# Kernel tuning notes

Hardware: AMD Instinct MI355X
Metric: run time of the kernel (lower is better)

The kernel has to match this reference:

```python
import jax, jax.numpy as jnp
import numpy as np

B, L, D = 8, 1024, 1024
H = 16
DPH = D // H  # 64
MAX_REL = 32  # relative position clip; vocab = 2*MAX_REL+1 (use_neg_dist=True)


def setup_inputs() -> dict:
    key = jax.random.key(0)
    ks = jax.random.split(key, 12)
    s = 1.0 / np.sqrt(D)
    return {
        "key": jax.random.normal(ks[0], (B, L, D), jnp.float32),
        "value": jax.random.normal(ks[1], (B, L, D), jnp.float32),
        "query": jax.random.normal(ks[2], (B, L, D), jnp.float32),
        "Wq": jax.random.normal(ks[3], (D, D), jnp.float32) * s,
        "bq": jnp.zeros((D,), jnp.float32),
        "Wk": jax.random.normal(ks[4], (D, D), jnp.float32) * s,
        "bk": jnp.zeros((D,), jnp.float32),
        "Wv": jax.random.normal(ks[5], (D, D), jnp.float32) * s,
        "bv": jnp.zeros((D,), jnp.float32),
        "Wo": jax.random.normal(ks[6], (D, D), jnp.float32) * s,
        "bo": jnp.zeros((D,), jnp.float32),
        "rel_emb": jax.random.normal(ks[7], (2 * MAX_REL + 1, DPH), jnp.float32) * 0.02,
    }


def reference(key, value, query, Wq, bq, Wk, bk, Wv, bv, Wo, bo, rel_emb):
    # shape: [B, L, D] -> [B, H, L, DPH]
    def shape(x):
        return x.reshape(B, L, H, DPH).transpose(0, 2, 1, 3)

    q = shape(query @ Wq.T + bq) / np.float32(np.sqrt(DPH))
    k = shape(key @ Wk.T + bk)
    v = shape(value @ Wv.T + bv)

    # relative position indices, clipped to [-MAX_REL, MAX_REL], shifted to [0, 2*MAX_REL]
    r = jnp.arange(L)
    dist = jnp.clip(r[None, :] - r[:, None], -MAX_REL, MAX_REL) + MAX_REL  # [L, L]
    rel = rel_emb[dist]  # [L, L, DPH]; same table for keys and values

    # scores = QK^T + Q . rel_keys  (relative_matmul with transpose=True)
    scores = jnp.einsum('bhqd,bhkd->bhqk', q, k) + jnp.einsum('bhqd,qkd->bhqk', q, rel)
    attn = jax.nn.softmax(scores.astype(jnp.float32), axis=-1).astype(q.dtype)

    # context = attn @ V + attn . rel_values (relative_matmul with transpose=False)
    ctx = jnp.einsum('bhqk,bhkd->bhqd', attn, v) + jnp.einsum('bhqk,qkd->bhqd', attn, rel)
    ctx = ctx.transpose(0, 2, 1, 3).reshape(B, L, D)
    out = ctx @ Wo.T + bo
    return out, attn
```

## Files before the change

### kernel.cpp

```cpp
#include <hip/hip_runtime.h>

typedef unsigned short u16;
typedef _Float16 f16;
typedef __attribute__((ext_vector_type(8))) _Float16 f16x8;
typedef __attribute__((ext_vector_type(4))) _Float16 f16x4;
typedef __attribute__((ext_vector_type(2))) _Float16 f16x2;
typedef __attribute__((ext_vector_type(4))) float f32x4;

#define MFMA16(acc, a, b) acc = __builtin_amdgcn_mfma_f32_16x16x32_f16(a, b, acc, 0, 0, 0)

__device__ __forceinline__ void gl2lds16(const void* g, void* l) {
  __builtin_amdgcn_global_load_lds(
      (const __attribute__((address_space(1))) void*)g,
      (__attribute__((address_space(3))) void*)l, 16, 0, 0);
}

__device__ __forceinline__ void cvt8(const float* __restrict__ src, f16* __restrict__ dst, int i) {
  const float* p = src + (size_t)i * 8;
  f32x4 a = *(const f32x4*)p;
  f32x4 b = *(const f32x4*)(p + 4);
  f16x8 o;
#pragma unroll
  for (int j = 0; j < 4; j++) {
    o[j] = (f16)a[j];
    o[j + 4] = (f16)b[j];
  }
  *(f16x8*)(dst + (size_t)i * 8) = o;
}

__global__ __launch_bounds__(256) void cvt_all(const float* __restrict__ Wq, const float* __restrict__ Wk,
                                               const float* __restrict__ Wv, const float* __restrict__ Wo,
                                               const float* __restrict__ rel, f16* __restrict__ f0,
                                               f16* __restrict__ f1, f16* __restrict__ f2,
                                               f16* __restrict__ f3, f16* __restrict__ fr) {
  const int NW = 131072;
  int i = blockIdx.x * 256 + threadIdx.x;
  if (i < NW) cvt8(Wq, f0, i);
  else if (i < 2 * NW) cvt8(Wk, f1, i - NW);
  else if (i < 3 * NW) cvt8(Wv, f2, i - 2 * NW);
  else if (i < 4 * NW) cvt8(Wo, f3, i - 3 * NW);
  else if (i < 4 * NW + 520) cvt8(rel, fr, i - 4 * NW);
}

__global__ __launch_bounds__(256) void gemm_qkv(const float* __restrict__ Aq, const float* __restrict__ Ak,
                                                const float* __restrict__ Av, const f16* __restrict__ W0,
                                                const f16* __restrict__ W1, const f16* __restrict__ W2,
                                                const float* __restrict__ b0, const float* __restrict__ b1,
                                                const float* __restrict__ b2, f16* __restrict__ O0,
                                                f16* __restrict__ O1, f16* __restrict__ O2) {
  int id = blockIdx.x;
  int which = id >> 9;
  int iid = id & 511;
  const float* A = (which == 0) ? Aq : (which == 1) ? Ak : Av;
  const f16* Wt = (which == 0) ? W0 : (which == 1) ? W1 : W2;
  const float* bias = (which == 0) ? b0 : (which == 1) ? b1 : b2;
  f16* out = (which == 0) ? O0 : (which == 1) ? O1 : O2;
  float scale = (which == 0) ? 0.125f : 1.0f;

  int m0 = (iid >> 3) << 7;
  int n0 = (iid & 7) << 7;
  int tid = threadIdx.x;
  int w = tid >> 6, lane = tid & 63, c = lane & 15, g = lane >> 4;
  int wm = (w >> 1) << 6, wn = (w & 1) << 6;

  __shared__ f16 As[128 * 32];
  __shared__ f16 Bs[128 * 32];

  f32x4 acc[4][4] = {};
  int ci0 = tid, ci1 = tid + 256;
  int r0 = ci0 >> 2, ks0 = (ci0 & 3) << 3;
  int r1 = ci1 >> 2, ks1 = (ci1 & 3) << 3;

  for (int k0 = 0; k0 < 1024; k0 += 32) {
    __syncthreads();
    gl2lds16(Wt + (size_t)(n0 + (ci0 >> 2)) * 1024 + k0 + ((ci0 & 3) << 3), Bs + w * 512);
    gl2lds16(Wt + (size_t)(n0 + (ci1 >> 2)) * 1024 + k0 + ((ci1 & 3) << 3), Bs + w * 512 + 2048);
    {
      const float* ap0 = A + (size_t)(m0 + r0) * 1024 + k0 + ks0;
      const float* ap1 = A + (size_t)(m0 + r1) * 1024 + k0 + ks1;
      f32x4 x0 = *(const f32x4*)ap0, x1 = *(const f32x4*)(ap0 + 4);
      f32x4 y0 = *(const f32x4*)ap1, y1 = *(const f32x4*)(ap1 + 4);
      f16x8 h0, h1;
#pragma unroll
      for (int j = 0; j < 4; j++) {
        h0[j] = (f16)x0[j];
        h0[j + 4] = (f16)x1[j];
        h1[j] = (f16)y0[j];
        h1[j + 4] = (f16)y1[j];
      }
      *(f16x8*)(As + (r0 << 5) + ks0) = h0;
      *(f16x8*)(As + (r1 << 5) + ks1) = h1;
    }
    __syncthreads();
    f16x8 af[4], bf[4];
#pragma unroll
    for (int mf = 0; mf < 4; mf++) af[mf] = *(const f16x8*)(As + ((wm + mf * 16 + c) << 5) + (g << 3));
#pragma unroll
    for (int nf = 0; nf < 4; nf++) bf[nf] = *(const f16x8*)(Bs + ((wn + nf * 16 + c) << 5) + (g << 3));
#pragma unroll
    for (int mf = 0; mf < 4; mf++)
#pragma unroll
      for (int nf = 0; nf < 4; nf++) MFMA16(acc[mf][nf], af[mf], bf[nf]);
  }

#pragma unroll
  for (int mf = 0; mf < 4; mf++)
#pragma unroll
    for (int nf = 0; nf < 4; nf++) {
      int row0 = m0 + wm + mf * 16 + (g << 2);
      int col = n0 + wn + nf * 16 + c;
      if (which == 2) {
        f16x4 vv;
#pragma unroll
        for (int r = 0; r < 4; r++) vv[r] = (f16)(acc[mf][nf][r] + bias[col]);
        size_t idx = (size_t)((row0 >> 10) * 16 + (col >> 6)) * 65536 + (size_t)(col & 63) * 1024 + (row0 & 1023);
        *(f16x4*)(out + idx) = vv;
      } else {
#pragma unroll
        for (int r = 0; r < 4; r++) {
          int row = row0 + r;
          size_t idx = (size_t)((row >> 10) * 16 + (col >> 6)) * 65536 + ((row & 1023) << 6) + (col & 63);
          out[idx] = (f16)((acc[mf][nf][r] + bias[col]) * scale);
        }
      }
    }
}

__global__ __launch_bounds__(256) void gemm_out(const f16* __restrict__ A, const f16* __restrict__ Wt,
                                                const float* __restrict__ bias, float* __restrict__ out) {
  int id = blockIdx.x;
  int m0 = (id >> 3) << 7;
  int n0 = (id & 7) << 7;
  int tid = threadIdx.x;
  int w = tid >> 6, lane = tid & 63, c = lane & 15, g = lane >> 4;
  int wm = (w >> 1) << 6, wn = (w & 1) << 6;

  __shared__ f16 As[128 * 32];
  __shared__ f16 Bs[128 * 32];

  f32x4 acc[4][4] = {};
  int ci0 = tid, ci1 = tid + 256;

  for (int k0 = 0; k0 < 1024; k0 += 32) {
    __syncthreads();
    gl2lds16(A + (size_t)(m0 + (ci0 >> 2)) * 1024 + k0 + ((ci0 & 3) << 3), As + w * 512);
    gl2lds16(A + (size_t)(m0 + (ci1 >> 2)) * 1024 + k0 + ((ci1 & 3) << 3), As + w * 512 + 2048);
    gl2lds16(Wt + (size_t)(n0 + (ci0 >> 2)) * 1024 + k0 + ((ci0 & 3) << 3), Bs + w * 512);
    gl2lds16(Wt + (size_t)(n0 + (ci1 >> 2)) * 1024 + k0 + ((ci1 & 3) << 3), Bs + w * 512 + 2048);
    __syncthreads();
    f16x8 af[4], bf[4];
#pragma unroll
    for (int mf = 0; mf < 4; mf++) af[mf] = *(const f16x8*)(As + ((wm + mf * 16 + c) << 5) + (g << 3));
#pragma unroll
    for (int nf = 0; nf < 4; nf++) bf[nf] = *(const f16x8*)(Bs + ((wn + nf * 16 + c) << 5) + (g << 3));
#pragma unroll
    for (int mf = 0; mf < 4; mf++)
#pragma unroll
      for (int nf = 0; nf < 4; nf++) MFMA16(acc[mf][nf], af[mf], bf[nf]);
  }

#pragma unroll
  for (int mf = 0; mf < 4; mf++)
#pragma unroll
    for (int nf = 0; nf < 4; nf++)
#pragma unroll
      for (int r = 0; r < 4; r++) {
        int row = m0 + wm + mf * 16 + (g << 2) + r;
        int col = n0 + wn + nf * 16 + c;
        out[(size_t)row * 1024 + col] = acc[mf][nf][r] + bias[col];
      }
}

__global__ __launch_bounds__(256) void attn_fused(const f16* __restrict__ Q, const f16* __restrict__ Km,
                                                  const f16* __restrict__ Vt, const f16* __restrict__ rel,
                                                  float* __restrict__ attn, f16* __restrict__ ctx) {
  int id = blockIdx.x;
  int sw = ((id & 7) << 10) + (id >> 3);
  int bh = sw >> 6;
  int q0 = (sw & 63) << 4;
  int b = bh >> 4, h = bh & 15;
  int tid = threadIdx.x;
  int w = tid >> 6, lane = tid & 63, c = lane & 15, g = lane >> 4;

  __shared__ float qrel_s[16 * 68];
  __shared__ float rmax[4][16], rsum[4][16], rlo[4][16], rhi[4][16];
  __shared__ float lo_s[16], hi_s[16];
  __shared__ f16 Pq[16][1032];
  __shared__ f16 rel_s[65 * 64];

  const f16* Qb = Q + ((size_t)bh << 16);
  const f16* Kb = Km + ((size_t)bh << 16);
  const f16* Vtb = Vt + ((size_t)bh << 16);

  for (int i = tid; i < 65 * 64; i += 256) rel_s[i] = rel[i];

  f16x8 aq0 = *(const f16x8*)(Qb + ((q0 + c) << 6) + (g << 3));
  f16x8 aq1 = *(const f16x8*)(Qb + ((q0 + c) << 6) + 32 + (g << 3));

  if (w == 0) {
#pragma unroll
    for (int tf = 0; tf < 5; tf++) {
      int t = tf * 16 + c;
      int tc = (t < 65) ? t : 0;
      f32x4 ar = {};
      f16x8 b0 = *(const f16x8*)(rel + (tc << 6) + (g << 3));
      f16x8 b1 = *(const f16x8*)(rel + (tc << 6) + 32 + (g << 3));
      MFMA16(ar, aq0, b0);
      MFMA16(ar, aq1, b1);
      if (t < 65) {
#pragma unroll
        for (int r = 0; r < 4; r++) qrel_s[((g << 2) + r) * 68 + t] = ar[r];
      }
    }
  }
  __syncthreads();

  float s[16][4];
  int kbase = w << 8;
#pragma unroll
  for (int f = 0; f < 16; f++) {
    int kcol = kbase + (f << 4) + c;
    f32x4 a4 = {};
    f16x8 b0 = *(const f16x8*)(Kb + (kcol << 6) + (g << 3));
    f16x8 b1 = *(const f16x8*)(Kb + (kcol << 6) + 32 + (g << 3));
    MFMA16(a4, aq0, b0);
    MFMA16(a4, aq1, b1);
#pragma unroll
    for (int r = 0; r < 4; r++) {
      int rowl = (g << 2) + r;
      int d = kcol - (q0 + rowl);
      int t = (d < -32 ? -32 : (d > 32 ? 32 : d)) + 32;
      s[f][r] = a4[r] + qrel_s[rowl * 68 + t];
    }
  }

  float m[4] = {-3.0e38f, -3.0e38f, -3.0e38f, -3.0e38f};
#pragma unroll
  for (int f = 0; f < 16; f++)
#pragma unroll
    for (int r = 0; r < 4; r++) m[r] = fmaxf(m[r], s[f][r]);
#pragma unroll
  for (int mk = 1; mk <= 8; mk <<= 1)
#pragma unroll
    for (int r = 0; r < 4; r++) m[r] = fmaxf(m[r], __shfl_xor(m[r], mk, 64));
  if (c == 0) {
#pragma unroll
    for (int r = 0; r < 4; r++) rmax[w][(g << 2) + r] = m[r];
  }
  __syncthreads();
  float gm[4];
#pragma unroll
  for (int r = 0; r < 4; r++) {
    int rowl = (g << 2) + r;
    gm[r] = fmaxf(fmaxf(rmax[0][rowl], rmax[1][rowl]), fmaxf(rmax[2][rowl], rmax[3][rowl]));
  }
  float sum[4] = {0, 0, 0, 0}, lo[4] = {0, 0, 0, 0}, hi[4] = {0, 0, 0, 0};
#pragma unroll
  for (int f = 0; f < 16; f++)
#pragma unroll
    for (int r = 0; r < 4; r++) {
      float p = __expf(s[f][r] - gm[r]);
      s[f][r] = p;
      sum[r] += p;
      int d = (kbase + (f << 4) + c) - (q0 + (g << 2) + r);
      if (d <= -32) lo[r] += p;
      if (d >= 32) hi[r] += p;
    }
#pragma unroll
  for (int mk = 1; mk <= 8; mk <<= 1)
#pragma unroll
    for (int r = 0; r < 4; r++) {
      sum[r] += __shfl_xor(sum[r], mk, 64);
      lo[r] += __shfl_xor(lo[r], mk, 64);
      hi[r] += __shfl_xor(hi[r], mk, 64);
    }
  if (c == 0) {
#pragma unroll
    for (int r = 0; r < 4; r++) {
      int rowl = (g << 2) + r;
      rsum[w][rowl] = sum[r];
      rlo[w][rowl] = lo[r];
      rhi[w][rowl] = hi[r];
    }
  }
  __syncthreads();
  float inv[4];
#pragma unroll
  for (int r = 0; r < 4; r++) {
    int rowl = (g << 2) + r;
    float tot = rsum[0][rowl] + rsum[1][rowl] + rsum[2][rowl] + rsum[3][rowl];
    inv[r] = 1.0f / tot;
  }
  if (w == 0 && c == 0) {
#pragma unroll
    for (int r = 0; r < 4; r++) {
      int rowl = (g << 2) + r;
      float l4 = rlo[0][rowl] + rlo[1][rowl] + rlo[2][rowl] + rlo[3][rowl];
      float h4 = rhi[0][rowl] + rhi[1][rowl] + rhi[2][rowl] + rhi[3][rowl];
      lo_s[rowl] = l4 * inv[r];
      hi_s[rowl] = h4 * inv[r];
    }
  }

#pragma unroll
  for (int f = 0; f < 16; f++) {
    int k = kbase + (f << 4) + c;
#pragma unroll
    for (int r = 0; r < 4; r++) Pq[(g << 2) + r][k] = (f16)(s[f][r] * inv[r]);
  }
  __syncthreads();

  {
    float* ab = attn + ((size_t)bh << 20) + ((size_t)q0 << 10);
    int k4 = tid << 2;
#pragma unroll
    for (int ch = 0; ch < 16; ch++) {
      f16x4 pv = *(const f16x4*)(&Pq[ch][k4]);
      f32x4 o;
#pragma unroll
      for (int j = 0; j < 4; j++) o[j] = (float)pv[j];
      *(f32x4*)(ab + ((size_t)ch << 10) + k4) = o;
    }
  }

  f32x4 pv0 = {}, pv1 = {};
  const f16* vrow = Vtb + (size_t)((w << 4) + c) * 1024;
#pragma unroll 4
  for (int kk = 0; kk < 1024; kk += 64) {
    f16x8 aV0 = *(const f16x8*)(vrow + kk + (g << 3));
    f16x8 bP0 = *(const f16x8*)(&Pq[c][kk + (g << 3)]);
    MFMA16(pv0, aV0, bP0);
    f16x8 aV1 = *(const f16x8*)(vrow + kk + 32 + (g << 3));
    f16x8 bP1 = *(const f16x8*)(&Pq[c][kk + 32 + (g << 3)]);
    MFMA16(pv1, aV1, bP1);
  }

  int qg = q0 + c;
  int d0 = (w << 4) + (g << 2);
  float cval[4];
  {
    f16x4 r0v = *(const f16x4*)(&rel_s[d0]);
    f16x4 r64v = *(const f16x4*)(&rel_s[64 * 64 + d0]);
#pragma unroll
    for (int r = 0; r < 4; r++)
      cval[r] = pv0[r] + pv1[r] + lo_s[c] * (float)r0v[r] + hi_s[c] * (float)r64v[r];
  }
  for (int t = 1; t < 64; t++) {
    int k = qg + t - 32;
    if (k >= 0 && k < 1024) {
      float pk = (float)Pq[c][k];
      f16x4 rv = *(const f16x4*)(&rel_s[t * 64 + d0]);
#pragma unroll
      for (int r = 0; r < 4; r++) cval[r] += pk * (float)rv[r];
    }
  }

#pragma unroll
  for (int r = 0; r < 4; r++) {
    ctx[(((size_t)(b << 10) + qg) << 10) + (h << 6) + d0 + r] = (f16)cval[r];
  }
}

extern "C" void kernel_launch(void* const* d_in, const int* in_sizes, int n_in, void* d_out, int out_size,
                              void* d_ws, size_t ws_size, hipStream_t stream) {
  const float* key = (const float*)d_in[0];
  const float* value = (const float*)d_in[1];
  const float* query = (const float*)d_in[2];
  const float* Wq = (const float*)d_in[3];
  const float* bq = (const float*)d_in[4];
  const float* Wk = (const float*)d_in[5];
  const float* bk = (const float*)d_in[6];
  const float* Wv = (const float*)d_in[7];
  const float* bv = (const float*)d_in[8];
  const float* Wo = (const float*)d_in[9];
  const float* bo = (const float*)d_in[10];
  const float* rel = (const float*)d_in[11];

  char* ws = (char*)d_ws;
  f16* ctx = (f16*)(ws);
  f16* Wf0 = (f16*)(ws);
  f16* Wf1 = (f16*)(ws + (2u << 20));
  f16* Wf2 = (f16*)(ws + (4u << 20));
  f16* Qw = (f16*)(ws + (16u << 20));
  f16* Kw = (f16*)(ws + (32u << 20));
  f16* Vw = (f16*)(ws + (48u << 20));
  f16* Wf3 = (f16*)(ws + (64u << 20));
  f16* relf = (f16*)(ws + (66u << 20));

  float* outp = (float*)d_out;
  float* attnp = outp + (size_t)8 * 1024 * 1024;

  dim3 blk(256);
  cvt_all<<<2051, blk, 0, stream>>>(Wq, Wk, Wv, Wo, rel, Wf0, Wf1, Wf2, Wf3, relf);
  gemm_qkv<<<1536, blk, 0, stream>>>(query, key, value, Wf0, Wf1, Wf2, bq, bk, bv, Qw, Kw, Vw);
  attn_fused<<<8192, blk, 0, stream>>>(Qw, Kw, Vw, relf, attnp, ctx);
  gemm_out<<<512, blk, 0, stream>>>(ctx, Wf3, bo, outp);
}
```

Before: 500.9 us.

## Prefetch K/V fragments, defer softmax normalization, swizzle P tile in LDS

Double-buffers K fragment loads in the score loop and keeps four V fragment pairs in flight during the PV loop, so global load latency overlaps with MFMA work. Unnormalized exponentials are written straight to a shared P tile that uses an XOR swizzle to avoid bank conflicts. The 1/sum scaling is deferred to the attn store and the final context write. The shared rel table is dropped in favour of global reads, and launch bounds request 4 blocks per CU, which may force register spills. Storing unnormalized probabilities in fp16 may slightly change accuracy.

Measured after the change: 673.1 us. +34.4%, slower.

```diff
diff --git a/kernel.cpp b/kernel.cpp
--- a/kernel.cpp
+++ b/kernel.cpp
@@ -4,7 +4,6 @@
 typedef _Float16 f16;
 typedef __attribute__((ext_vector_type(8))) _Float16 f16x8;
 typedef __attribute__((ext_vector_type(4))) _Float16 f16x4;
-typedef __attribute__((ext_vector_type(2))) _Float16 f16x2;
 typedef __attribute__((ext_vector_type(4))) float f32x4;
 
 #define MFMA16(acc, a, b) acc = __builtin_amdgcn_mfma_f32_16x16x32_f16(a, b, acc, 0, 0, 0)
@@ -171,9 +170,9 @@
       }
 }
 
-__global__ __launch_bounds__(256) void attn_fused(const f16* __restrict__ Q, const f16* __restrict__ Km,
-                                                  const f16* __restrict__ Vt, const f16* __restrict__ rel,
-                                                  float* __restrict__ attn, f16* __restrict__ ctx) {
+__global__ __launch_bounds__(256, 4) void attn_fused(const f16* __restrict__ Q, const f16* __restrict__ Km,
+                                                     const f16* __restrict__ Vt, const f16* __restrict__ rel,
+                                                     float* __restrict__ attn, f16* __restrict__ ctx) {
   int id = blockIdx.x;
   int sw = ((id & 7) << 10) + (id >> 3);
   int bh = sw >> 6;
@@ -184,15 +183,12 @@
 
   __shared__ float qrel_s[16 * 68];
   __shared__ float rmax[4][16], rsum[4][16], rlo[4][16], rhi[4][16];
-  __shared__ float lo_s[16], hi_s[16];
-  __shared__ f16 Pq[16][1032];
-  __shared__ f16 rel_s[65 * 64];
+  __shared__ float lo_s[16], hi_s[16], inv_s[16];
+  __shared__ f16 Pq[16 * 1024];
 
   const f16* Qb = Q + ((size_t)bh << 16);
   const f16* Kb = Km + ((size_t)bh << 16);
   const f16* Vtb = Vt + ((size_t)bh << 16);
-
-  for (int i = tid; i < 65 * 64; i += 256) rel_s[i] = rel[i];
 
   f16x8 aq0 = *(const f16x8*)(Qb + ((q0 + c) << 6) + (g << 3));
   f16x8 aq1 = *(const f16x8*)(Qb + ((q0 + c) << 6) + 32 + (g << 3));
@@ -217,22 +213,33 @@
 
   float s[16][4];
   int kbase = w << 8;
-#pragma unroll
-  for (int f = 0; f < 16; f++) {
-    int kcol = kbase + (f << 4) + c;
-    f32x4 a4 = {};
-    f16x8 b0 = *(const f16x8*)(Kb + (kcol << 6) + (g << 3));
-    f16x8 b1 = *(const f16x8*)(Kb + (kcol << 6) + 32 + (g << 3));
-    MFMA16(a4, aq0, b0);
-    MFMA16(a4, aq1, b1);
-#pragma unroll
-    for (int r = 0; r < 4; r++) {
-      int rowl = (g << 2) + r;
-      int d = kcol - (q0 + rowl);
-      int t = (d < -32 ? -32 : (d > 32 ? 32 : d)) + 32;
-      s[f][r] = a4[r] + qrel_s[rowl * 68 + t];
-    }
-  }
+  f16x8 kA0, kA1, kB0, kB1;
+#define KLOAD(K0, K1, F)                                              \
+  {                                                                   \
+    int kcol_ = kbase + ((F) << 4) + c;                               \
+    K0 = *(const f16x8*)(Kb + (kcol_ << 6) + (g << 3));               \
+    K1 = *(const f16x8*)(Kb + (kcol_ << 6) + 32 + (g << 3));          \
+  }
+#define SC_STEP(F, K0, K1)                                            \
+  {                                                                   \
+    f32x4 a4 = {};                                                    \
+    MFMA16(a4, aq0, K0);                                              \
+    MFMA16(a4, aq1, K1);                                              \
+    if ((F) + 2 < 16) KLOAD(K0, K1, (F) + 2)                          \
+    int kcol_ = kbase + ((F) << 4) + c;                               \
+    _Pragma("unroll") for (int r = 0; r < 4; r++) {                   \
+      int rowl_ = (g << 2) + r;                                       \
+      int d_ = kcol_ - (q0 + rowl_);                                  \
+      int t_ = (d_ < -32 ? -32 : (d_ > 32 ? 32 : d_)) + 32;           \
+      s[F][r] = a4[r] + qrel_s[rowl_ * 68 + t_];                      \
+    }                                                                 \
+  }
+  KLOAD(kA0, kA1, 0)
+  KLOAD(kB0, kB1, 1)
+  SC_STEP(0, kA0, kA1) SC_STEP(1, kB0, kB1) SC_STEP(2, kA0, kA1) SC_STEP(3, kB0, kB1)
+  SC_STEP(4, kA0, kA1) SC_STEP(5, kB0, kB1) SC_STEP(6, kA0, kA1) SC_STEP(7, kB0, kB1)
+  SC_STEP(8, kA0, kA1) SC_STEP(9, kB0, kB1) SC_STEP(10, kA0, kA1) SC_STEP(11, kB0, kB1)
+  SC_STEP(12, kA0, kA1) SC_STEP(13, kB0, kB1) SC_STEP(14, kA0, kA1) SC_STEP(15, kB0, kB1)
 
   float m[4] = {-3.0e38f, -3.0e38f, -3.0e38f, -3.0e38f};
 #pragma unroll
@@ -254,18 +261,22 @@
     int rowl = (g << 2) + r;
     gm[r] = fmaxf(fmaxf(rmax[0][rowl], rmax[1][rowl]), fmaxf(rmax[2][rowl], rmax[3][rowl]));
   }
+
   float sum[4] = {0, 0, 0, 0}, lo[4] = {0, 0, 0, 0}, hi[4] = {0, 0, 0, 0};
 #pragma unroll
-  for (int f = 0; f < 16; f++)
+  for (int f = 0; f < 16; f++) {
+    int k = kbase + (f << 4) + c;
 #pragma unroll
     for (int r = 0; r < 4; r++) {
       float p = __expf(s[f][r] - gm[r]);
-      s[f][r] = p;
       sum[r] += p;
-      int d = (kbase + (f << 4) + c) - (q0 + (g << 2) + r);
+      int rowl = (g << 2) + r;
+      int d = k - (q0 + rowl);
       if (d <= -32) lo[r] += p;
       if (d >= 32) hi[r] += p;
-    }
+      *(f16*)((char*)Pq + (rowl << 11) + (((k) << 1) ^ ((rowl & 7) << 4))) = (f16)p;
+    }
+  }
 #pragma unroll
   for (int mk = 1; mk <= 8; mk <<= 1)
 #pragma unroll
@@ -284,80 +295,76 @@
     }
   }
   __syncthreads();
-  float inv[4];
-#pragma unroll
-  for (int r = 0; r < 4; r++) {
-    int rowl = (g << 2) + r;
-    float tot = rsum[0][rowl] + rsum[1][rowl] + rsum[2][rowl] + rsum[3][rowl];
-    inv[r] = 1.0f / tot;
-  }
-  if (w == 0 && c == 0) {
-#pragma unroll
-    for (int r = 0; r < 4; r++) {
-      int rowl = (g << 2) + r;
-      float l4 = rlo[0][rowl] + rlo[1][rowl] + rlo[2][rowl] + rlo[3][rowl];
-      float h4 = rhi[0][rowl] + rhi[1][rowl] + rhi[2][rowl] + rhi[3][rowl];
-      lo_s[rowl] = l4 * inv[r];
-      hi_s[rowl] = h4 * inv[r];
-    }
-  }
-
-#pragma unroll
-  for (int f = 0; f < 16; f++) {
-    int k = kbase + (f << 4) + c;
-#pragma unroll
-    for (int r = 0; r < 4; r++) Pq[(g << 2) + r][k] = (f16)(s[f][r] * inv[r]);
+  if (tid < 16) {
+    float tot = rsum[0][tid] + rsum[1][tid] + rsum[2][tid] + rsum[3][tid];
+    inv_s[tid] = 1.0f / tot;
+    lo_s[tid] = rlo[0][tid] + rlo[1][tid] + rlo[2][tid] + rlo[3][tid];
+    hi_s[tid] = rhi[0][tid] + rhi[1][tid] + rhi[2][tid] + rhi[3][tid];
   }
   __syncthreads();
+
+  const f16* vrow = Vtb + (size_t)((w << 4) + c) * 1024;
+  f16x8 vA0, vA1, vB0, vB1, vC0, vC1, vD0, vD1;
+#define VLOAD(V0, V1, J)                                    \
+  {                                                         \
+    V0 = *(const f16x8*)(vrow + ((J) << 6) + (g << 3));     \
+    V1 = *(const f16x8*)(vrow + ((J) << 6) + 32 + (g << 3));\
+  }
+  VLOAD(vA0, vA1, 0) VLOAD(vB0, vB1, 1) VLOAD(vC0, vC1, 2) VLOAD(vD0, vD1, 3)
 
   {
     float* ab = attn + ((size_t)bh << 20) + ((size_t)q0 << 10);
     int k4 = tid << 2;
 #pragma unroll
     for (int ch = 0; ch < 16; ch++) {
-      f16x4 pv = *(const f16x4*)(&Pq[ch][k4]);
+      f16x4 pv = *(const f16x4*)((char*)Pq + (ch << 11) + (((k4) << 1) ^ ((ch & 7) << 4)));
+      float iv = inv_s[ch];
       f32x4 o;
 #pragma unroll
-      for (int j = 0; j < 4; j++) o[j] = (float)pv[j];
+      for (int j = 0; j < 4; j++) o[j] = (float)pv[j] * iv;
       *(f32x4*)(ab + ((size_t)ch << 10) + k4) = o;
     }
   }
 
   f32x4 pv0 = {}, pv1 = {};
-  const f16* vrow = Vtb + (size_t)((w << 4) + c) * 1024;
-#pragma unroll 4
-  for (int kk = 0; kk < 1024; kk += 64) {
-    f16x8 aV0 = *(const f16x8*)(vrow + kk + (g << 3));
-    f16x8 bP0 = *(const f16x8*)(&Pq[c][kk + (g << 3)]);
-    MFMA16(pv0, aV0, bP0);
-    f16x8 aV1 = *(const f16x8*)(vrow + kk + 32 + (g << 3));
-    f16x8 bP1 = *(const f16x8*)(&Pq[c][kk + 32 + (g << 3)]);
-    MFMA16(pv1, aV1, bP1);
-  }
+#define BPQ(KK) (*(const f16x8*)((char*)Pq + (c << 11) + ((((KK) + (g << 3)) << 1) ^ ((c & 7) << 4))))
+#define PV_STEP(J, V0, V1)                         \
+  {                                                \
+    f16x8 bp0_ = BPQ((J) << 6);                    \
+    f16x8 bp1_ = BPQ(((J) << 6) + 32);             \
+    MFMA16(pv0, V0, bp0_);                         \
+    MFMA16(pv1, V1, bp1_);                         \
+    if ((J) + 4 < 16) VLOAD(V0, V1, (J) + 4)       \
+  }
+  PV_STEP(0, vA0, vA1) PV_STEP(1, vB0, vB1) PV_STEP(2, vC0, vC1) PV_STEP(3, vD0, vD1)
+  PV_STEP(4, vA0, vA1) PV_STEP(5, vB0, vB1) PV_STEP(6, vC0, vC1) PV_STEP(7, vD0, vD1)
+  PV_STEP(8, vA0, vA1) PV_STEP(9, vB0, vB1) PV_STEP(10, vC0, vC1) PV_STEP(11, vD0, vD1)
+  PV_STEP(12, vA0, vA1) PV_STEP(13, vB0, vB1) PV_STEP(14, vC0, vC1) PV_STEP(15, vD0, vD1)
 
   int qg = q0 + c;
   int d0 = (w << 4) + (g << 2);
   float cval[4];
   {
-    f16x4 r0v = *(const f16x4*)(&rel_s[d0]);
-    f16x4 r64v = *(const f16x4*)(&rel_s[64 * 64 + d0]);
+    f16x4 r0v = *(const f16x4*)(rel + d0);
+    f16x4 r64v = *(const f16x4*)(rel + 64 * 64 + d0);
+    float l4 = lo_s[c], h4 = hi_s[c];
 #pragma unroll
     for (int r = 0; r < 4; r++)
-      cval[r] = pv0[r] + pv1[r] + lo_s[c] * (float)r0v[r] + hi_s[c] * (float)r64v[r];
+      cval[r] = pv0[r] + pv1[r] + l4 * (float)r0v[r] + h4 * (float)r64v[r];
   }
   for (int t = 1; t < 64; t++) {
     int k = qg + t - 32;
     if (k >= 0 && k < 1024) {
-      float pk = (float)Pq[c][k];
-      f16x4 rv = *(const f16x4*)(&rel_s[t * 64 + d0]);
+      float pk = (float)*(const f16*)((char*)Pq + (c << 11) + (((k) << 1) ^ ((c & 7) << 4)));
+      f16x4 rv = *(const f16x4*)(rel + t * 64 + d0);
 #pragma unroll
       for (int r = 0; r < 4; r++) cval[r] += pk * (float)rv[r];
     }
   }
-
+  float ivc = inv_s[c];
 #pragma unroll
   for (int r = 0; r < 4; r++) {
-    ctx[(((size_t)(b << 10) + qg) << 10) + (h << 6) + d0 + r] = (f16)cval[r];
+    ctx[(((size_t)(b << 10) + qg) << 10) + (h << 6) + d0 + r] = (f16)(cval[r] * ivc);
   }
 }
 
```
